# Kernel optimization log

Measured on AMD Instinct MI355X. Metric: run time of the kernel, lower is better.

The kernel has to match this reference:

```python
import jax, jax.numpy as jnp
import numpy as np
from jax import lax

H = 256  # hidden_size


def _conv1d(x, w, b):
    # x: (N, Cin, L), w: (Cout, Cin, K) -> (N, Cout, L-K+1), VALID, stride 1
    y = lax.conv_general_dilated(x, w, window_strides=(1,), padding='VALID',
                                 dimension_numbers=('NCH', 'OIH', 'NCH'))
    return y + b[None, :, None]


def _gru_dir(x, Wih, Whh, bih, bhh):
    # x: (L, N, H). Torch GRU cell equations.
    L, N, _ = x.shape
    gi = jnp.einsum('lnh,gh->lng', x, Wih) + bih  # (L, N, 3H) precomputed input gates
    h0 = jnp.zeros((N, H), x.dtype)

    def step(h, gi_t):
        gh = h @ Whh.T + bhh                       # (N, 3H)
        ir, iz, inn = jnp.split(gi_t, 3, axis=-1)
        hr, hz, hn = jnp.split(gh, 3, axis=-1)
        r = jax.nn.sigmoid(ir + hr)
        z = jax.nn.sigmoid(iz + hz)
        n = jnp.tanh(inn + r * hn)
        h_new = (1.0 - z) * n + z * h
        return h_new, h_new

    hT, ys = lax.scan(step, h0, gi)
    return ys, hT  # (L, N, H), (N, H)


def setup_inputs() -> dict:
    key = jax.random.key(0)
    ks = jax.random.split(key, 14)
    N, C, L = 32, 13, 4096
    s = 0.1
    inp = {
        'X': jax.random.normal(ks[0], (N, C, L), jnp.float32),
        'W1': jax.random.normal(ks[1], (H // 2, C, 3), jnp.float32) * s,
        'b1': jax.random.normal(ks[2], (H // 2,), jnp.float32) * s,
        'W2': jax.random.normal(ks[3], (H, H // 2, 3), jnp.float32) * s,
        'b2': jax.random.normal(ks[4], (H,), jnp.float32) * s,
        'Wih_f': jax.random.normal(ks[5], (3 * H, H), jnp.float32) * s,
        'Whh_f': jax.random.normal(ks[6], (3 * H, H), jnp.float32) * s,
        'bih_f': jax.random.normal(ks[7], (3 * H,), jnp.float32) * s,
        'bhh_f': jax.random.normal(ks[8], (3 * H,), jnp.float32) * s,
        'Wih_b': jax.random.normal(ks[9], (3 * H, H), jnp.float32) * s,
        'Whh_b': jax.random.normal(ks[10], (3 * H, H), jnp.float32) * s,
        'bih_b': jax.random.normal(ks[11], (3 * H,), jnp.float32) * s,
        'bhh_b': jax.random.normal(ks[12], (3 * H,), jnp.float32) * s,
    }
    return inp


def reference(X, W1, b1, W2, b2, Wih_f, Whh_f, bih_f, bhh_f,
              Wih_b, Whh_b, bih_b, bhh_b):
    # dropouts are identity in eval mode; N>1 so squeeze() is a no-op
    x = _conv1d(X, W1, b1)           # (N, H/2, L-2)
    x = _conv1d(x, W2, b2)           # (N, H,   L-4)
    x = x[:, :, ::2]                 # MaxPool1d(kernel=1, stride=2) == stride-2 subsample
    x = jnp.transpose(x, (2, 0, 1))  # (L', N, H)

    out_f, hT_f = _gru_dir(x, Wih_f, Whh_f, bih_f, bhh_f)
    # backward direction: reverse time, scan, reverse outputs
    out_b_rev, hT_b = _gru_dir(x[::-1], Wih_b, Whh_b, bih_b, bhh_b)
    out_b = out_b_rev[::-1]

    # original: fwd + flip(bwd along FEATURE axis), averaged, ReLU (faithful to np.flip(axis=-1))
    comb = jax.nn.relu((out_f + out_b[:, :, ::-1]) * 0.5)  # (L', N, H)
    hidden_last = hT_b[None]                                # hidden[-1].unsqueeze(0): (1, N, H)
    return comb, hidden_last
```

## Files before the change

### kernel.cpp

```cpp
#include <hip/hip_runtime.h>
#include <hip/hip_fp16.h>
#include <cstdint>
#include <cstddef>

#define L_SEQ 2046
#define NBATCH 32
#define HID 256
#define M_PAD 65536

typedef _Float16 h2vec __attribute__((ext_vector_type(2)));
typedef _Float16 half8 __attribute__((ext_vector_type(8)));
typedef float f32x4 __attribute__((ext_vector_type(4)));

static __device__ __forceinline__ uint32_t pack2(float a, float b) {
  __half2 h = __floats2half2_rn(a, b);
  return __builtin_bit_cast(uint32_t, h);
}

__global__ void k_conv_im2col(const float* __restrict__ X,
                              const float* __restrict__ W1,
                              const float* __restrict__ b1,
                              __half* __restrict__ A1h) {
  int j   = threadIdx.x;
  int row = blockIdx.x;
  int l2 = row >> 5, n = row & 31;
  float v = 0.f;
  if (l2 < L_SEQ) {
    int ci = j / 3;
    int k  = j - 3 * ci;
    int p  = 2 * l2 + k;
    const float* xb = X + (size_t)n * 13 * 4096 + p;
    const float* w  = W1 + ci * 39;
    float acc = b1[ci];
#pragma unroll
    for (int c = 0; c < 13; c++) {
      const float* xp = xb + (size_t)c * 4096;
      acc += xp[0] * w[3*c+0] + xp[1] * w[3*c+1] + xp[2] * w[3*c+2];
    }
    v = acc;
  }
  A1h[(size_t)row * 384 + j] = __float2half(v);
}

__global__ __launch_bounds__(256, 4) void k_gemm_h(
    const __half* __restrict__ A, const float* __restrict__ B,
    const float* __restrict__ bias, __half* __restrict__ C,
    int K, int ldC, int col_off) {
  __shared__ float As[32][132];
  __shared__ float Bs[32][132];
  const int tid = threadIdx.x;
  const int m_blk = blockIdx.x * 128;
  const int n_blk = blockIdx.y * 128;
  const int tx = tid & 15, ty = tid >> 4;
  const int m0 = tx * 8, n0 = ty * 8;
  const int sr = tid >> 3;
  const int sc = 4 * (tid & 7);
  const int ar = tid >> 1;
  const int ak = 16 * (tid & 1);

  float acc[8][8];
#pragma unroll
  for (int i = 0; i < 8; i++)
#pragma unroll
    for (int j = 0; j < 8; j++) acc[i][j] = 0.f;

  for (int kc = 0; kc < K; kc += 32) {
    const __half* ap = A + (size_t)(m_blk + ar) * K + kc + ak;
    uint4 h0 = *(const uint4*)(ap);
    uint4 h1 = *(const uint4*)(ap + 8);
    {
      uint32_t hw[8] = {h0.x, h0.y, h0.z, h0.w, h1.x, h1.y, h1.z, h1.w};
#pragma unroll
      for (int p = 0; p < 8; p++) {
        float2 f = __half22float2(__builtin_bit_cast(__half2, hw[p]));
        As[ak + 2*p    ][ar] = f.x;
        As[ak + 2*p + 1][ar] = f.y;
      }
    }
#pragma unroll
    for (int i = 0; i < 4; i++) {
      int r = i * 32 + sr;
      float4 vb = *(const float4*)(B + (size_t)(n_blk + r) * K + kc + sc);
      Bs[sc+0][r] = vb.x; Bs[sc+1][r] = vb.y; Bs[sc+2][r] = vb.z; Bs[sc+3][r] = vb.w;
    }
    __syncthreads();
#pragma unroll 8
    for (int k = 0; k < 32; k++) {
      float a[8], b[8];
      *(float4*)(a)     = *(const float4*)&As[k][m0];
      *(float4*)(a + 4) = *(const float4*)&As[k][m0 + 4];
      *(float4*)(b)     = *(const float4*)&Bs[k][n0];
      *(float4*)(b + 4) = *(const float4*)&Bs[k][n0 + 4];
#pragma unroll
      for (int i = 0; i < 8; i++)
#pragma unroll
        for (int j = 0; j < 8; j++) acc[i][j] += a[i] * b[j];
    }
    __syncthreads();
  }
  float bj[8];
#pragma unroll
  for (int j = 0; j < 8; j++) bj[j] = bias[n_blk + n0 + j];
#pragma unroll
  for (int i = 0; i < 8; i++) {
    uint4 o;
    o.x = pack2(acc[i][0] + bj[0], acc[i][1] + bj[1]);
    o.y = pack2(acc[i][2] + bj[2], acc[i][3] + bj[3]);
    o.z = pack2(acc[i][4] + bj[4], acc[i][5] + bj[5]);
    o.w = pack2(acc[i][6] + bj[6], acc[i][7] + bj[7]);
    *(uint4*)(C + (size_t)(m_blk + m0 + i) * ldC + col_off + n_blk + n0) = o;
  }
}

__global__ void k_packw(const float* __restrict__ Whh_f,
                        const float* __restrict__ Whh_b,
                        uint4* __restrict__ Wpk) {
  int idx = blockIdx.x * 256 + threadIdx.x;
  int d   = idx / 24576;
  int r2  = idx - d * 24576;
  int tl  = r2 >> 9;
  int tid = r2 & 511;
  int w = tid >> 6, lane = tid & 63;
  int group = tl >> 3, kc = tl & 7;
  int row = w * 96 + group * 16 + (lane & 15);
  int kb  = kc * 32 + (lane >> 4) * 8;
  const float* W = d ? Whh_b : Whh_f;
  const float* src = W + (size_t)row * 256 + kb;
  uint4 o;
  o.x = pack2(src[0], src[1]);
  o.y = pack2(src[2], src[3]);
  o.z = pack2(src[4], src[5]);
  o.w = pack2(src[6], src[7]);
  Wpk[(size_t)idx] = o;
}

__global__ __attribute__((amdgpu_flat_work_group_size(512, 512),
                          amdgpu_waves_per_eu(2, 2)))
void k_gru(
    const __half* __restrict__ gih, const uint4* __restrict__ Wpk,
    const float* __restrict__ bhh_f, const float* __restrict__ bhh_b,
    float* __restrict__ outF, __half* __restrict__ outBh,
    float* __restrict__ hT) {
  const int blk = blockIdx.x;
  const int dir = blk >> 5;
  const int n   = blk & 31;
  const int tid = threadIdx.x;
  const int lane = tid & 63;
  const int w    = tid >> 6;
  const int g    = tid;

  uint4 wv[48];
  {
    const uint4* wp = Wpk + (size_t)dir * 24576 + tid;
#pragma unroll
    for (int j = 0; j < 48; j++) wv[j] = wp[j * 512];
#pragma unroll
    for (int j = 0; j < 48; j++) {
      asm volatile("" : "+v"(wv[j].x), "+v"(wv[j].y), "+v"(wv[j].z), "+v"(wv[j].w));
    }
  }
  const float* bhh = dir ? bhh_b : bhh_f;
  float bh0 = 0.f, bh1 = 0.f, bh2 = 0.f;
  if (tid < 256) { bh0 = bhh[g]; bh1 = bhh[256 + g]; bh2 = bhh[512 + g]; }

  __shared__ __align__(16) __half hs[2][256];
  __shared__ __align__(16) float  pa[768];
  if (tid < 128) ((uint32_t*)hs)[tid] = 0u;
  float hp = 0.f;

  const __half* gr = gih + ((size_t)(dir ? (size_t)(L_SEQ - 1) * NBATCH : 0) + n) * 1536
                         + dir * 768 + g;
  const ptrdiff_t gstep = dir ? -(ptrdiff_t)(NBATCH * 1536) : (ptrdiff_t)(NBATCH * 1536);
  __half pi0 = __float2half(0.f), pi1 = pi0, pi2 = pi0;
  if (tid < 256) { pi0 = gr[0]; pi1 = gr[256]; pi2 = gr[512]; }

  const int qoff = (lane >> 4) << 4;
  const int rowb = w * 96 + (lane >> 4) * 4;
  __syncthreads();

  for (int t = 0; t < L_SEQ; t++) {
    const char* hcur = (const char*)hs[t & 1];
    half8 bf[8];
#pragma unroll
    for (int kc = 0; kc < 8; kc++)
      bf[kc] = __builtin_bit_cast(half8, *(const uint4*)(hcur + kc * 64 + qoff));

    f32x4 acc[6];
#pragma unroll
    for (int g6 = 0; g6 < 6; g6++) acc[g6] = (f32x4){0.f, 0.f, 0.f, 0.f};
#pragma unroll
    for (int kc = 0; kc < 8; kc++)
#pragma unroll
      for (int g6 = 0; g6 < 6; g6++)
        acc[g6] = __builtin_amdgcn_mfma_f32_16x16x32_f16(
            __builtin_bit_cast(half8, wv[g6 * 8 + kc]), bf[kc], acc[g6], 0, 0, 0);

    if ((lane & 15) == 0) {
#pragma unroll
      for (int g6 = 0; g6 < 6; g6++)
        *(f32x4*)&pa[rowb + g6 * 16] = acc[g6];
    }
    __syncthreads();

    if (tid < 256) {
      float hr = pa[g]       + bh0;
      float hz = pa[256 + g] + bh1;
      float hn = pa[512 + g] + bh2;
      float ir  = __half2float(pi0);
      float iz  = __half2float(pi1);
      float inn = __half2float(pi2);
      float rr = 1.f / (1.f + __expf(-(ir + hr)));
      float zz = 1.f / (1.f + __expf(-(iz + hz)));
      float e  = __expf(2.f * (inn + rr * hn));
      float nn = 1.f - 2.f / (e + 1.f);
      float hnew = (1.f - zz) * nn + zz * hp;
      hp = hnew;
      __half hh = __float2half(hnew);
      hs[(t + 1) & 1][g] = hh;
      const int l = dir ? (L_SEQ - 1 - t) : t;
      uint32_t oi = ((uint32_t)l * NBATCH + n) * HID + g;
      if (dir == 0) outF[oi] = hnew;
      else          outBh[oi] = hh;
      gr += gstep;
      if (t + 1 < L_SEQ) { pi0 = gr[0]; pi1 = gr[256]; pi2 = gr[512]; }
    }
    __syncthreads();
  }
  if (dir == 1 && tid < 256) hT[n * HID + g] = hp;
}

__global__ void k_combine(float* __restrict__ outF,
                          const __half* __restrict__ outBh) {
  int idx = blockIdx.x * 256 + threadIdx.x;
  int c = idx & 255;
  float v = 0.5f * (outF[idx] + __half2float(outBh[idx + 255 - 2 * c]));
  outF[idx] = v > 0.f ? v : 0.f;
}

extern "C" void kernel_launch(void* const* d_in, const int* in_sizes, int n_in,
                              void* d_out, int out_size, void* d_ws, size_t ws_size,
                              hipStream_t stream) {
  const float* X     = (const float*)d_in[0];
  const float* W1    = (const float*)d_in[1];
  const float* b1    = (const float*)d_in[2];
  const float* W2    = (const float*)d_in[3];
  const float* b2    = (const float*)d_in[4];
  const float* Wih_f = (const float*)d_in[5];
  const float* Whh_f = (const float*)d_in[6];
  const float* bih_f = (const float*)d_in[7];
  const float* bhh_f = (const float*)d_in[8];
  const float* Wih_b = (const float*)d_in[9];
  const float* Whh_b = (const float*)d_in[10];
  const float* bih_b = (const float*)d_in[11];
  const float* bhh_b = (const float*)d_in[12];

  char* wsb = (char*)d_ws;
  __half* gih   = (__half*)(wsb);
  __half* A1h   = (__half*)(wsb + 201326592);
  __half* outBh = (__half*)(wsb + 201326592);
  uint4*  Wpk   = (uint4*)(wsb + 234848768);

  float*  outF  = (float*)d_out;
  __half* xsubh = (__half*)d_out;
  float*  hT    = outF + (size_t)L_SEQ * NBATCH * HID;

  k_conv_im2col<<<dim3(M_PAD), 384, 0, stream>>>(X, W1, b1, A1h);
  k_gemm_h<<<dim3(512, 2), 256, 0, stream>>>(A1h, W2, b2, xsubh, 384, 256, 0);
  k_packw<<<dim3(192), 256, 0, stream>>>(Whh_f, Whh_b, Wpk);
  k_gemm_h<<<dim3(512, 6), 256, 0, stream>>>(xsubh, Wih_f, bih_f, gih, 256, 1536, 0);
  k_gemm_h<<<dim3(512, 6), 256, 0, stream>>>(xsubh, Wih_b, bih_b, gih, 256, 1536, 768);
  k_gru<<<dim3(64), 512, 0, stream>>>(gih, Wpk, bhh_f, bhh_b, outF, outBh, hT);
  k_combine<<<dim3(65472), 256, 0, stream>>>(outF, outBh);
}
```

Baseline: 3.778 ms.

## Batch 16 sequences per GRU block to fill MFMA columns and fuse gate math

The recurrent GRU kernel now processes 16 batch elements per block, so the 16x16 MFMA columns hold distinct sequences rather than duplicating one hidden vector. Gate nonlinearities are computed directly from accumulator registers, removing the shared-memory staging of partial products and one barrier per step. Recurrent weights are repacked so each wave owns matching r/z/n rows, and the r/z hidden biases are folded into the input-projection GEMM bias via a small precompute kernel. Only 4 blocks run, which leaves most of the GPU idle, and more elementwise work falls on each thread.

```diff
diff --git a/kernel.cpp b/kernel.cpp
--- a/kernel.cpp
+++ b/kernel.cpp
@@ -112,6 +112,17 @@
   }
 }
 
+__global__ void k_biasc(const float* __restrict__ bih_f, const float* __restrict__ bhh_f,
+                        const float* __restrict__ bih_b, const float* __restrict__ bhh_b,
+                        float* __restrict__ biasc) {
+  int i = blockIdx.x * 256 + threadIdx.x;
+  int d = i / 768;
+  int o = i - d * 768;
+  const float* bi = d ? bih_b : bih_f;
+  const float* bh = d ? bhh_b : bhh_f;
+  biasc[i] = bi[o] + (o < 512 ? bh[o] : 0.f);
+}
+
 __global__ void k_packw(const float* __restrict__ Whh_f,
                         const float* __restrict__ Whh_b,
                         uint4* __restrict__ Wpk) {
@@ -121,8 +132,9 @@
   int tl  = r2 >> 9;
   int tid = r2 & 511;
   int w = tid >> 6, lane = tid & 63;
-  int group = tl >> 3, kc = tl & 7;
-  int row = w * 96 + group * 16 + (lane & 15);
+  int g6 = tl >> 3, kc = tl & 7;
+  int gate = g6 >> 1, hi = g6 & 1;
+  int row = gate * 256 + w * 32 + hi * 16 + (lane & 15);
   int kb  = kc * 32 + (lane >> 4) * 8;
   const float* W = d ? Whh_b : Whh_f;
   const float* src = W + (size_t)row * 256 + kb;
@@ -142,12 +154,14 @@
     float* __restrict__ outF, __half* __restrict__ outBh,
     float* __restrict__ hT) {
   const int blk = blockIdx.x;
-  const int dir = blk >> 5;
-  const int n   = blk & 31;
+  const int dir = blk >> 1;
+  const int nb  = (blk & 1) * 16;
   const int tid = threadIdx.x;
   const int lane = tid & 63;
-  const int w    = tid >> 6;
-  const int g    = tid;
+  const int w = tid >> 6;
+  const int c = lane & 15;
+  const int quad = lane >> 4;
+  const int hbase0 = w * 32 + quad * 4;
 
   uint4 wv[48];
   {
@@ -155,35 +169,43 @@
 #pragma unroll
     for (int j = 0; j < 48; j++) wv[j] = wp[j * 512];
 #pragma unroll
-    for (int j = 0; j < 48; j++) {
+    for (int j = 0; j < 48; j++)
       asm volatile("" : "+v"(wv[j].x), "+v"(wv[j].y), "+v"(wv[j].z), "+v"(wv[j].w));
-    }
-  }
+  }
+
   const float* bhh = dir ? bhh_b : bhh_f;
-  float bh0 = 0.f, bh1 = 0.f, bh2 = 0.f;
-  if (tid < 256) { bh0 = bhh[g]; bh1 = bhh[256 + g]; bh2 = bhh[512 + g]; }
-
-  __shared__ __align__(16) __half hs[2][256];
-  __shared__ __align__(16) float  pa[768];
-  if (tid < 128) ((uint32_t*)hs)[tid] = 0u;
-  float hp = 0.f;
-
-  const __half* gr = gih + ((size_t)(dir ? (size_t)(L_SEQ - 1) * NBATCH : 0) + n) * 1536
-                         + dir * 768 + g;
+  float bn[2][4];
+#pragma unroll
+  for (int hi = 0; hi < 2; hi++)
+#pragma unroll
+    for (int r = 0; r < 4; r++) bn[hi][r] = bhh[512 + hbase0 + hi * 16 + r];
+
+  __shared__ __align__(16) __half hs[2][16][272];
+  for (int i = tid; i < 2 * 16 * 136; i += 512) ((uint32_t*)hs)[i] = 0u;
+  float hp[2][4] = {{0.f, 0.f, 0.f, 0.f}, {0.f, 0.f, 0.f, 0.f}};
+
+  const int l0 = dir ? (L_SEQ - 1) : 0;
+  const __half* gbase = gih + ((size_t)l0 * NBATCH + nb + c) * 1536 + dir * 768;
   const ptrdiff_t gstep = dir ? -(ptrdiff_t)(NBATCH * 1536) : (ptrdiff_t)(NBATCH * 1536);
-  __half pi0 = __float2half(0.f), pi1 = pi0, pi2 = pi0;
-  if (tid < 256) { pi0 = gr[0]; pi1 = gr[256]; pi2 = gr[512]; }
-
-  const int qoff = (lane >> 4) << 4;
-  const int rowb = w * 96 + (lane >> 4) * 4;
+  uint2 pg[3][2];
+#pragma unroll
+  for (int gate = 0; gate < 3; gate++)
+#pragma unroll
+    for (int hi = 0; hi < 2; hi++)
+      pg[gate][hi] = *(const uint2*)(gbase + gate * 256 + hbase0 + hi * 16);
+
+  const ptrdiff_t ostep = dir ? -(ptrdiff_t)(NBATCH * HID) : (ptrdiff_t)(NBATCH * HID);
+  float*  ofp = outF  + ((size_t)l0 * NBATCH + nb + c) * HID + hbase0;
+  __half* obp = outBh + ((size_t)l0 * NBATCH + nb + c) * HID + hbase0;
+
   __syncthreads();
 
   for (int t = 0; t < L_SEQ; t++) {
-    const char* hcur = (const char*)hs[t & 1];
+    const __half* hrow = &hs[t & 1][c][0];
     half8 bf[8];
 #pragma unroll
     for (int kc = 0; kc < 8; kc++)
-      bf[kc] = __builtin_bit_cast(half8, *(const uint4*)(hcur + kc * 64 + qoff));
+      bf[kc] = __builtin_bit_cast(half8, *(const uint4*)(hrow + kc * 32 + quad * 8));
 
     f32x4 acc[6];
 #pragma unroll
@@ -195,38 +217,61 @@
         acc[g6] = __builtin_amdgcn_mfma_f32_16x16x32_f16(
             __builtin_bit_cast(half8, wv[g6 * 8 + kc]), bf[kc], acc[g6], 0, 0, 0);
 
-    if ((lane & 15) == 0) {
-#pragma unroll
-      for (int g6 = 0; g6 < 6; g6++)
-        *(f32x4*)&pa[rowb + g6 * 16] = acc[g6];
+    __half* hwrow = &hs[(t + 1) & 1][c][0];
+#pragma unroll
+    for (int hi = 0; hi < 2; hi++) {
+      float2 irA = __half22float2(__builtin_bit_cast(__half2, pg[0][hi].x));
+      float2 irB = __half22float2(__builtin_bit_cast(__half2, pg[0][hi].y));
+      float2 izA = __half22float2(__builtin_bit_cast(__half2, pg[1][hi].x));
+      float2 izB = __half22float2(__builtin_bit_cast(__half2, pg[1][hi].y));
+      float2 inA = __half22float2(__builtin_bit_cast(__half2, pg[2][hi].x));
+      float2 inB = __half22float2(__builtin_bit_cast(__half2, pg[2][hi].y));
+      float ir[4]  = {irA.x, irA.y, irB.x, irB.y};
+      float iz[4]  = {izA.x, izA.y, izB.x, izB.y};
+      float inn[4] = {inA.x, inA.y, inB.x, inB.y};
+      float hv[4];
+#pragma unroll
+      for (int r = 0; r < 4; r++) {
+        float a_r = acc[0 + hi][r];
+        float a_z = acc[2 + hi][r];
+        float a_n = acc[4 + hi][r];
+        float rr = 1.f / (1.f + __expf(-(ir[r] + a_r)));
+        float zz = 1.f / (1.f + __expf(-(iz[r] + a_z)));
+        float e  = __expf(2.f * (inn[r] + rr * (a_n + bn[hi][r])));
+        float nn = 1.f - 2.f / (e + 1.f);
+        float hnew = (1.f - zz) * nn + zz * hp[hi][r];
+        hp[hi][r] = hnew;
+        hv[r] = hnew;
+      }
+      uint2 hpk;
+      hpk.x = pack2(hv[0], hv[1]);
+      hpk.y = pack2(hv[2], hv[3]);
+      *(uint2*)(hwrow + hbase0 + hi * 16) = hpk;
+      if (dir == 0) {
+        *(float4*)(ofp + hi * 16) = make_float4(hv[0], hv[1], hv[2], hv[3]);
+      } else {
+        *(uint2*)(obp + hi * 16) = hpk;
+      }
+    }
+    gbase += gstep;
+    ofp += ostep;
+    obp += ostep;
+    if (t + 1 < L_SEQ) {
+#pragma unroll
+      for (int gate = 0; gate < 3; gate++)
+#pragma unroll
+        for (int hi = 0; hi < 2; hi++)
+          pg[gate][hi] = *(const uint2*)(gbase + gate * 256 + hbase0 + hi * 16);
     }
     __syncthreads();
-
-    if (tid < 256) {
-      float hr = pa[g]       + bh0;
-      float hz = pa[256 + g] + bh1;
-      float hn = pa[512 + g] + bh2;
-      float ir  = __half2float(pi0);
-      float iz  = __half2float(pi1);
-      float inn = __half2float(pi2);
-      float rr = 1.f / (1.f + __expf(-(ir + hr)));
-      float zz = 1.f / (1.f + __expf(-(iz + hz)));
-      float e  = __expf(2.f * (inn + rr * hn));
-      float nn = 1.f - 2.f / (e + 1.f);
-      float hnew = (1.f - zz) * nn + zz * hp;
-      hp = hnew;
-      __half hh = __float2half(hnew);
-      hs[(t + 1) & 1][g] = hh;
-      const int l = dir ? (L_SEQ - 1 - t) : t;
-      uint32_t oi = ((uint32_t)l * NBATCH + n) * HID + g;
-      if (dir == 0) outF[oi] = hnew;
-      else          outBh[oi] = hh;
-      gr += gstep;
-      if (t + 1 < L_SEQ) { pi0 = gr[0]; pi1 = gr[256]; pi2 = gr[512]; }
-    }
-    __syncthreads();
-  }
-  if (dir == 1 && tid < 256) hT[n * HID + g] = hp;
+  }
+
+  if (dir == 1) {
+#pragma unroll
+    for (int hi = 0; hi < 2; hi++)
+      *(float4*)(hT + (size_t)(nb + c) * HID + hbase0 + hi * 16) =
+          make_float4(hp[hi][0], hp[hi][1], hp[hi][2], hp[hi][3]);
+  }
 }
 
 __global__ void k_combine(float* __restrict__ outF,
@@ -259,6 +304,7 @@
   __half* A1h   = (__half*)(wsb + 201326592);
   __half* outBh = (__half*)(wsb + 201326592);
   uint4*  Wpk   = (uint4*)(wsb + 234848768);
+  float*  biasc = (float*)(wsb + 235635200);
 
   float*  outF  = (float*)d_out;
   __half* xsubh = (__half*)d_out;
@@ -267,8 +313,9 @@
   k_conv_im2col<<<dim3(M_PAD), 384, 0, stream>>>(X, W1, b1, A1h);
   k_gemm_h<<<dim3(512, 2), 256, 0, stream>>>(A1h, W2, b2, xsubh, 384, 256, 0);
   k_packw<<<dim3(192), 256, 0, stream>>>(Whh_f, Whh_b, Wpk);
-  k_gemm_h<<<dim3(512, 6), 256, 0, stream>>>(xsubh, Wih_f, bih_f, gih, 256, 1536, 0);
-  k_gemm_h<<<dim3(512, 6), 256, 0, stream>>>(xsubh, Wih_b, bih_b, gih, 256, 1536, 768);
-  k_gru<<<dim3(64), 512, 0, stream>>>(gih, Wpk, bhh_f, bhh_b, outF, outBh, hT);
+  k_biasc<<<dim3(6), 256, 0, stream>>>(bih_f, bhh_f, bih_b, bhh_b, biasc);
+  k_gemm_h<<<dim3(512, 6), 256, 0, stream>>>(xsubh, Wih_f, biasc, gih, 256, 1536, 0);
+  k_gemm_h<<<dim3(512, 6), 256, 0, stream>>>(xsubh, Wih_b, biasc + 768, gih, 256, 1536, 768);
+  k_gru<<<dim3(4), 512, 0, stream>>>(gih, Wpk, bhh_f, bhh_b, outF, outBh, hT);
   k_combine<<<dim3(65472), 256, 0, stream>>>(outF, outBh);
 }
```

Result: slower. 10.77 ms (+185.2%).
